# Kernel optimization log

Hardware: AMD Instinct MI355X
Metric: run time of the kernel (lower is better)

Reference implementation:

```python
import jax, jax.numpy as jnp
import numpy as np

B, S, H, NH, FF = 16, 1024, 768, 12, 3072
D = H // NH  # 64
EPS = 1e-12


def layer_norm(x, g, b):
    mu = jnp.mean(x, axis=-1, keepdims=True)
    var = jnp.mean(jnp.square(x - mu), axis=-1, keepdims=True)
    return (x - mu) * jax.lax.rsqrt(var + EPS) * g + b


def setup_inputs() -> dict:
    key = jax.random.key(0)
    ks = jax.random.split(key, 16)
    w = lambda k, shape: (jax.random.normal(k, shape, jnp.float32) * 0.02)
    return {
        "features": jax.random.normal(ks[0], (B, S, H), jnp.float32),
        "attention_mask": jnp.zeros((B, S), jnp.float32),  # additive mask
        "wq": w(ks[1], (H, H)), "bq": jnp.zeros((H,), jnp.float32),
        "wk": w(ks[2], (H, H)), "bk": jnp.zeros((H,), jnp.float32),
        "wv": w(ks[3], (H, H)), "bv": jnp.zeros((H,), jnp.float32),
        "wo": w(ks[4], (H, H)), "bo": jnp.zeros((H,), jnp.float32),
        "ln1_g": jnp.ones((H,), jnp.float32), "ln1_b": jnp.zeros((H,), jnp.float32),
        "w1": w(ks[5], (H, FF)), "b1": jnp.zeros((FF,), jnp.float32),
        "w2": w(ks[6], (FF, H)), "b2": jnp.zeros((H,), jnp.float32),
        "ln2_g": jnp.ones((H,), jnp.float32), "ln2_b": jnp.zeros((H,), jnp.float32),
        "wp": w(ks[7], (H, H)), "bp": jnp.zeros((H,), jnp.float32),
        "wm": w(ks[8], (H, 1)), "bm": jnp.zeros((1,), jnp.float32),
    }


def reference(features, attention_mask, wq, bq, wk, bk, wv, bv, wo, bo,
              ln1_g, ln1_b, w1, b1, w2, b2, ln2_g, ln2_b, wp, bp, wm, bm):
    mask = attention_mask[:, None, None, :]  # [B,1,1,S]

    def split_heads(x):  # [B,S,H] -> [B,NH,S,D]
        return x.reshape(B, S, NH, D).transpose(0, 2, 1, 3)

    q = split_heads(features @ wq + bq)
    k = split_heads(features @ wk + bk)
    v = split_heads(features @ wv + bv)

    scores = jnp.einsum("bhqd,bhkd->bhqk", q, k) / np.sqrt(D).astype(np.float32)
    probs = jax.nn.softmax(scores + mask, axis=-1)  # dropout is identity (eval)
    ctx = jnp.einsum("bhqk,bhkd->bhqd", probs, v)
    ctx = ctx.transpose(0, 2, 1, 3).reshape(B, S, H)

    attn_out = layer_norm(ctx @ wo + bo + features, ln1_g, ln1_b)
    ffn = jax.nn.gelu(attn_out @ w1 + b1, approximate=False) @ w2 + b2
    hidden = layer_norm(ffn + attn_out, ln2_g, ln2_b)

    pooled = jnp.tanh(hidden[:, 0] @ wp + bp)  # BertPooler on [CLS]
    cls = (pooled @ wm + bm).squeeze()  # [B]
    return cls
```

## Files before the change

### kernel.cpp

```cpp
#include <hip/hip_runtime.h>
#include <math.h>

namespace {

constexpr int B  = 16;
constexpr int S  = 1024;
constexpr int H  = 768;
constexpr int NH = 12;
constexpr int DH = 64;
constexpr int FF = 3072;
constexpr int XSPL = 32;
constexpr float EPS = 1e-12f;

__device__ __forceinline__ float waveReduceSum(float v) {
#pragma unroll
    for (int d = 1; d < 64; d <<= 1) v += __shfl_xor(v, d);
    return v;
}

__device__ __forceinline__ float blockReduceSum768(float v, float* red) {
    const int lane = threadIdx.x & 63;
    const int wid  = threadIdx.x >> 6;
    v = waveReduceSum(v);
    __syncthreads();
    if (lane == 0) red[wid] = v;
    __syncthreads();
    float s = 0.f;
#pragma unroll
    for (int w = 0; w < 12; ++w) s += red[w];
    return s;
}

template <int K, int ISPL, int N>
__global__ __launch_bounds__(256) void gemm_partial(
        const float* __restrict__ A, int lda, int jtOfsA,
        const float* __restrict__ W, float* __restrict__ part) {
    constexpr int IR = K / ISPL;
    __shared__ float Asl[B * IR];
    const int jt  = blockIdx.x;
    const int sp  = blockIdx.y;
    const int i0  = sp * IR;
    const int tid = threadIdx.x;

    for (int e = tid; e < B * IR; e += 256) {
        const int b = e / IR, ii = e % IR;
        Asl[e] = A[(size_t)b * lda + (size_t)jt * jtOfsA + i0 + ii];
    }
    __syncthreads();

    const int jl = tid & 63;
    const int bg = tid >> 6;
    const int j  = jt * 64 + jl;
    const float* wp_ = W + (size_t)i0 * N + j;
    const float* a0 = Asl + (bg * 4 + 0) * IR;
    const float* a1 = Asl + (bg * 4 + 1) * IR;
    const float* a2 = Asl + (bg * 4 + 2) * IR;
    const float* a3 = Asl + (bg * 4 + 3) * IR;
    float acc0 = 0.f, acc1 = 0.f, acc2 = 0.f, acc3 = 0.f;
#pragma unroll
    for (int ii = 0; ii < IR; ++ii) {
        const float w = wp_[(size_t)ii * N];
        acc0 += w * a0[ii];
        acc1 += w * a1[ii];
        acc2 += w * a2[ii];
        acc3 += w * a3[ii];
    }
    float* pp = part + ((size_t)sp * B) * N + j;
    pp[(size_t)(bg * 4 + 0) * N] = acc0;
    pp[(size_t)(bg * 4 + 1) * N] = acc1;
    pp[(size_t)(bg * 4 + 2) * N] = acc2;
    pp[(size_t)(bg * 4 + 3) * N] = acc3;
}

template <int K, int ISPL, int N, int RED>
__global__ __launch_bounds__(256) void gemm_partial_red(
        const float* __restrict__ Ain, const float* __restrict__ bias,
        const float* __restrict__ W, float* __restrict__ part) {
    constexpr int IR = K / ISPL;
    __shared__ float Asl[B * IR];
    const int jt  = blockIdx.x;
    const int sp  = blockIdx.y;
    const int i0  = sp * IR;
    const int tid = threadIdx.x;

    for (int e = tid; e < B * IR; e += 256) {
        const int b = e / IR, ii = e % IR;
        float v = bias[i0 + ii];
#pragma unroll
        for (int sp2 = 0; sp2 < RED; ++sp2)
            v += Ain[((size_t)sp2 * B + b) * K + i0 + ii];
        Asl[e] = v;
    }
    __syncthreads();

    const int jl = tid & 63;
    const int bg = tid >> 6;
    const int j  = jt * 64 + jl;
    const float* wp_ = W + (size_t)i0 * N + j;
    const float* a0 = Asl + (bg * 4 + 0) * IR;
    const float* a1 = Asl + (bg * 4 + 1) * IR;
    const float* a2 = Asl + (bg * 4 + 2) * IR;
    const float* a3 = Asl + (bg * 4 + 3) * IR;
    float acc0 = 0.f, acc1 = 0.f, acc2 = 0.f, acc3 = 0.f;
#pragma unroll
    for (int ii = 0; ii < IR; ++ii) {
        const float w = wp_[(size_t)ii * N];
        acc0 += w * a0[ii];
        acc1 += w * a1[ii];
        acc2 += w * a2[ii];
        acc3 += w * a3[ii];
    }
    float* pp = part + ((size_t)sp * B) * N + j;
    pp[(size_t)(bg * 4 + 0) * N] = acc0;
    pp[(size_t)(bg * 4 + 1) * N] = acc1;
    pp[(size_t)(bg * 4 + 2) * N] = acc2;
    pp[(size_t)(bg * 4 + 3) * N] = acc3;
}

template <int K, int ISPL, int N, int RED>
__global__ __launch_bounds__(256) void gemm_partial_red_gelu(
        const float* __restrict__ Ain, const float* __restrict__ bias,
        const float* __restrict__ W, float* __restrict__ part) {
    constexpr int IR = K / ISPL;
    __shared__ float Asl[B * IR];
    const int jt  = blockIdx.x;
    const int sp  = blockIdx.y;
    const int i0  = sp * IR;
    const int tid = threadIdx.x;

    for (int e = tid; e < B * IR; e += 256) {
        const int b = e / IR, ii = e % IR;
        float v = bias[i0 + ii];
#pragma unroll
        for (int sp2 = 0; sp2 < RED; ++sp2)
            v += Ain[((size_t)sp2 * B + b) * K + i0 + ii];
        Asl[e] = 0.5f * v * (1.0f + erff(v * 0.70710678118654752440f));
    }
    __syncthreads();

    const int jl = tid & 63;
    const int bg = tid >> 6;
    const int j  = jt * 64 + jl;
    const float* wp_ = W + (size_t)i0 * N + j;
    const float* a0 = Asl + (bg * 4 + 0) * IR;
    const float* a1 = Asl + (bg * 4 + 1) * IR;
    const float* a2 = Asl + (bg * 4 + 2) * IR;
    const float* a3 = Asl + (bg * 4 + 3) * IR;
    float acc0 = 0.f, acc1 = 0.f, acc2 = 0.f, acc3 = 0.f;
#pragma unroll 32
    for (int ii = 0; ii < IR; ++ii) {
        const float w = wp_[(size_t)ii * N];
        acc0 += w * a0[ii];
        acc1 += w * a1[ii];
        acc2 += w * a2[ii];
        acc3 += w * a3[ii];
    }
    float* pp = part + ((size_t)sp * B) * N + j;
    pp[(size_t)(bg * 4 + 0) * N] = acc0;
    pp[(size_t)(bg * 4 + 1) * N] = acc1;
    pp[(size_t)(bg * 4 + 2) * N] = acc2;
    pp[(size_t)(bg * 4 + 3) * N] = acc3;
}

template <int ISPL>
__global__ __launch_bounds__(256) void gemm_xpart(
        const float* __restrict__ xpart, const float* __restrict__ psum,
        const float* __restrict__ W, float* __restrict__ part) {
    constexpr int IR = H / ISPL;
    __shared__ float Asl[B * IR];
    __shared__ float rinvl[B];
    const int jt  = blockIdx.x;
    const int sp  = blockIdx.y;
    const int i0  = sp * IR;
    const int tid = threadIdx.x;

    if (tid < B) {
        float s = 0.f;
#pragma unroll
        for (int kt = 0; kt < XSPL; ++kt)
            s += psum[((size_t)(tid * XSPL + kt)) * NH + jt];
        rinvl[tid] = 1.0f / s;
    }
    __syncthreads();

    for (int e = tid; e < B * IR; e += 256) {
        const int bb = e / IR, ii = e % IR;
        float v = 0.f;
#pragma unroll
        for (int s2 = 0; s2 < XSPL; ++s2)
            v += xpart[(((size_t)(bb * XSPL + s2)) * NH + jt) * H + i0 + ii];
        Asl[e] = v * rinvl[bb];
    }
    __syncthreads();

    const int jl = tid & 63;
    const int bg = tid >> 6;
    const int j  = jt * 64 + jl;
    const float* wp_ = W + (size_t)i0 * H + j;
    const float* a0 = Asl + (bg * 4 + 0) * IR;
    const float* a1 = Asl + (bg * 4 + 1) * IR;
    const float* a2 = Asl + (bg * 4 + 2) * IR;
    const float* a3 = Asl + (bg * 4 + 3) * IR;
    float acc0 = 0.f, acc1 = 0.f, acc2 = 0.f, acc3 = 0.f;
#pragma unroll
    for (int ii = 0; ii < IR; ++ii) {
        const float w = wp_[(size_t)ii * H];
        acc0 += w * a0[ii];
        acc1 += w * a1[ii];
        acc2 += w * a2[ii];
        acc3 += w * a3[ii];
    }
    float* pp = part + ((size_t)sp * B) * H + j;
    pp[(size_t)(bg * 4 + 0) * H] = acc0;
    pp[(size_t)(bg * 4 + 1) * H] = acc1;
    pp[(size_t)(bg * 4 + 2) * H] = acc2;
    pp[(size_t)(bg * 4 + 3) * H] = acc3;
}

__global__ __launch_bounds__(256) void qu_kernel(
        const float* __restrict__ x, const float* __restrict__ wq,
        const float* __restrict__ bq, const float* __restrict__ wk,
        const float* __restrict__ bk,
        float* __restrict__ u, float* __restrict__ constk) {
    const int b = blockIdx.x / NH, h = blockIdx.x % NH;
    __shared__ float qh[DH];
    __shared__ float red[4][DH];
    const int tid = threadIdx.x;
    const int d = tid & 63, seg = tid >> 6;

    {
        const float* xr  = x + (size_t)b * S * H;
        const float* wqp = wq + (size_t)(seg * 192) * H + h * DH + d;
        float acc = 0.f;
#pragma unroll 8
        for (int i = 0; i < 192; ++i)
            acc += xr[seg * 192 + i] * wqp[(size_t)i * H];
        red[seg][d] = acc;
    }
    __syncthreads();
    if (tid < DH)
        qh[tid] = bq[h * DH + tid] + red[0][tid] + red[1][tid] + red[2][tid] + red[3][tid];
    __syncthreads();
    if (tid < DH) {
        float v = bk[h * DH + tid] * qh[tid];
        v = waveReduceSum(v);
        if (tid == 0) constk[b * NH + h] = v;
    }

    const int jj = tid & 3, iq = tid >> 2;
    const float4* qv = (const float4*)qh;
    float4 q4[4];
#pragma unroll
    for (int c = 0; c < 4; ++c) q4[c] = qv[jj * 4 + c];
#pragma unroll 4
    for (int ir = 0; ir < 12; ++ir) {
        const int i = ir * 64 + iq;
        const float4* wr = (const float4*)(wk + (size_t)i * H + h * DH);
        float s = 0.f;
#pragma unroll
        for (int c = 0; c < 4; ++c) {
            const float4 w = wr[jj * 4 + c];
            s += w.x * q4[c].x + w.y * q4[c].y + w.z * q4[c].z + w.w * q4[c].w;
        }
        s += __shfl_xor(s, 1);
        s += __shfl_xor(s, 2);
        if (jj == 0) u[((size_t)(b * NH + h)) * H + i] = s;
    }
}

__global__ __launch_bounds__(256, 2) void score_xbar_kernel(
        const float* __restrict__ x, const float* __restrict__ u,
        const float* __restrict__ constk, const float* __restrict__ mask,
        float* __restrict__ psum, float* __restrict__ xpart) {
    const int b  = blockIdx.x;
    const int kt = blockIdx.y;
    __shared__ __align__(16) float ul[NH * H];
    __shared__ float ck[NH];
    __shared__ float wsum[4][NH];
    __shared__ __align__(16) float el[32][NH];
    const int tid = threadIdx.x;
    {
        const float4* ug = (const float4*)(u + (size_t)b * NH * H);
        float4* ul4 = (float4*)ul;
        for (int e = tid; e < NH * H / 4; e += 256) ul4[e] = ug[e];
        if (tid < NH) ck[tid] = constk[b * NH + tid];
    }
    __syncthreads();

    const int jj = tid & 15, kk = tid >> 4;
    const int k0 = kt * 32 + kk * 2;
    float4 xv0[12], xv1[12];
    {
        const float4* xr0 = (const float4*)(x + ((size_t)b * S + k0) * H);
        const float4* xr1 = (const float4*)(x + ((size_t)b * S + k0 + 1) * H);
#pragma unroll
        for (int t = 0; t < 12; ++t) { xv0[t] = xr0[jj + 16 * t]; xv1[t] = xr1[jj + 16 * t]; }
    }
    const float4* ul4 = (const float4*)ul;
    float acc0[NH], acc1[NH];
#pragma unroll
    for (int h = 0; h < NH; ++h) {
        float a0 = 0.f, a1 = 0.f;
#pragma unroll
        for (int t = 0; t < 12; ++t) {
            const float4 uv = ul4[h * 192 + jj + 16 * t];
            a0 += xv0[t].x * uv.x + xv0[t].y * uv.y + xv0[t].z * uv.z + xv0[t].w * uv.w;
            a1 += xv1[t].x * uv.x + xv1[t].y * uv.y + xv1[t].z * uv.z + xv1[t].w * uv.w;
        }
        acc0[h] = a0; acc1[h] = a1;
    }
#pragma unroll
    for (int h = 0; h < NH; ++h) {
#pragma unroll
        for (int d = 1; d < 16; d <<= 1) {
            acc0[h] += __shfl_xor(acc0[h], d);
            acc1[h] += __shfl_xor(acc1[h], d);
        }
    }
    const float mk0 = mask[b * S + k0];
    const float mk1 = mask[b * S + k0 + 1];
    float e0[NH], e1[NH], ps[NH];
#pragma unroll
    for (int h = 0; h < NH; ++h) {
        e0[h] = expf(acc0[h] * 0.125f + ck[h] + mk0);
        e1[h] = expf(acc1[h] * 0.125f + ck[h] + mk1);
        ps[h] = e0[h] + e1[h];
    }
    if (jj == 0) {
#pragma unroll
        for (int h = 0; h < NH; ++h) {
            el[kk * 2 + 0][h] = e0[h];
            el[kk * 2 + 1][h] = e1[h];
        }
    }
#pragma unroll
    for (int h = 0; h < NH; ++h) {
        ps[h] += __shfl_xor(ps[h], 16);
        ps[h] += __shfl_xor(ps[h], 32);
    }
    const int wid = tid >> 6;
    if ((tid & 63) == 0) {
#pragma unroll
        for (int h = 0; h < NH; ++h) wsum[wid][h] = ps[h];
    }
    __syncthreads();
    if (tid < NH)
        psum[((size_t)(b * XSPL + kt)) * NH + tid] =
            wsum[0][tid] + wsum[1][tid] + wsum[2][tid] + wsum[3][tid];

    float accx[3][NH];
#pragma unroll
    for (int c = 0; c < 3; ++c)
#pragma unroll
        for (int h = 0; h < NH; ++h) accx[c][h] = 0.f;
    const float* xb = x + ((size_t)b * S + (size_t)kt * 32) * H;
#pragma unroll 8
    for (int k = 0; k < 32; ++k) {
        const float xs0 = xb[(size_t)k * H + tid];
        const float xs1 = xb[(size_t)k * H + tid + 256];
        const float xs2 = xb[(size_t)k * H + tid + 512];
#pragma unroll
        for (int h = 0; h < NH; ++h) {
            const float ee = el[k][h];
            accx[0][h] += ee * xs0;
            accx[1][h] += ee * xs1;
            accx[2][h] += ee * xs2;
        }
    }
    float* op = xpart + ((size_t)(b * XSPL + kt)) * NH * H + tid;
#pragma unroll
    for (int h = 0; h < NH; ++h) {
        op[(size_t)h * H +   0] = accx[0][h];
        op[(size_t)h * H + 256] = accx[1][h];
        op[(size_t)h * H + 512] = accx[2][h];
    }
}

template <int ISPL>
__global__ __launch_bounds__(768) void ln_kernel(
        const float* __restrict__ part, const float* __restrict__ bias,
        const float* __restrict__ resid, int residStride,
        const float* __restrict__ g, const float* __restrict__ bet,
        float* __restrict__ out) {
    __shared__ float red[12];
    const int b = blockIdx.x, j = threadIdx.x;
    float v = bias[j] + resid[(size_t)b * residStride + j];
#pragma unroll
    for (int sp = 0; sp < ISPL; ++sp) v += part[((size_t)sp * B + b) * H + j];
    const float mu = blockReduceSum768(v, red) * (1.0f / H);
    const float d  = v - mu;
    const float var = blockReduceSum768(d * d, red) * (1.0f / H);
    out[(size_t)b * H + j] = d * rsqrtf(var + EPS) * g[j] + bet[j];
}

template <int ISPL>
__global__ __launch_bounds__(768) void cls_kernel(
        const float* __restrict__ part, const float* __restrict__ bp,
        const float* __restrict__ wm, const float* __restrict__ bm,
        float* __restrict__ out) {
    __shared__ float red[12];
    const int b = blockIdx.x, j = threadIdx.x;
    float v = bp[j];
#pragma unroll
    for (int sp = 0; sp < ISPL; ++sp) v += part[((size_t)sp * B + b) * H + j];
    v = tanhf(v);
    const float s = blockReduceSum768(v * wm[j], red);
    if (j == 0) out[b] = s + bm[0];
}

}

extern "C" void kernel_launch(void* const* d_in, const int* in_sizes, int n_in,
                              void* d_out, int out_size, void* d_ws, size_t ws_size,
                              hipStream_t stream) {
    const float* x    = (const float*)d_in[0];
    const float* mask = (const float*)d_in[1];
    const float* wq   = (const float*)d_in[2];
    const float* bq   = (const float*)d_in[3];
    const float* wk   = (const float*)d_in[4];
    const float* bk   = (const float*)d_in[5];
    const float* wv   = (const float*)d_in[6];
    const float* bv   = (const float*)d_in[7];
    const float* wo   = (const float*)d_in[8];
    const float* bo   = (const float*)d_in[9];
    const float* ln1g = (const float*)d_in[10];
    const float* ln1b = (const float*)d_in[11];
    const float* w1   = (const float*)d_in[12];
    const float* b1   = (const float*)d_in[13];
    const float* w2   = (const float*)d_in[14];
    const float* b2   = (const float*)d_in[15];
    const float* ln2g = (const float*)d_in[16];
    const float* ln2b = (const float*)d_in[17];
    const float* wp   = (const float*)d_in[18];
    const float* bp   = (const float*)d_in[19];
    const float* wm   = (const float*)d_in[20];
    const float* bm   = (const float*)d_in[21];
    float* out = (float*)d_out;

    float* ws = (float*)d_ws;
    size_t o = 0;
    float* u        = ws + o; o += (size_t)B * NH * H;
    float* constk   = ws + o; o += 256;
    float* psum     = ws + o; o += (size_t)B * XSPL * NH;
    float* attn_out = ws + o; o += (size_t)B * H;
    float* hidden   = ws + o; o += (size_t)B * H;
    float* arena    = ws + o;
    float* xpart     = arena;
    float* ctx_part  = arena + (size_t)XSPL * B * NH * H;
    float* wo_part   = ctx_part + (size_t)24 * B * H;
    float* ffn1_part = arena;
    float* ffn2_part = arena + (size_t)24 * B * FF;
    float* pool_part = arena;
    (void)ws_size; (void)in_sizes; (void)n_in; (void)out_size;

    qu_kernel<<<B * NH, 256, 0, stream>>>(x, wq, bq, wk, bk, u, constk);

    score_xbar_kernel<<<dim3(B, S / 32), 256, 0, stream>>>(x, u, constk, mask, psum, xpart);

    gemm_xpart<24><<<dim3(12, 24), 256, 0, stream>>>(xpart, psum, wv, ctx_part);

    gemm_partial_red<H, 24, H, 24><<<dim3(12, 24), 256, 0, stream>>>(ctx_part, bv, wo, wo_part);
    ln_kernel<24><<<B, 768, 0, stream>>>(wo_part, bo, x, S * H, ln1g, ln1b, attn_out);

    gemm_partial<H, 24, FF><<<dim3(48, 24), 256, 0, stream>>>(attn_out, H, 0, w1, ffn1_part);
    gemm_partial_red_gelu<FF, 48, H, 24><<<dim3(12, 48), 256, 0, stream>>>(ffn1_part, b1, w2, ffn2_part);
    ln_kernel<48><<<B, 768, 0, stream>>>(ffn2_part, b2, attn_out, H, ln2g, ln2b, hidden);

    gemm_partial<H, 24, H><<<dim3(12, 24), 256, 0, stream>>>(hidden, H, 0, wp, pool_part);
    cls_kernel<24><<<B, 768, 0, stream>>>(pool_part, bp, wm, bm, out);
}
```

Baseline: 217.2 us.

## Split CLS query projection into split-K GEMM, fuse pooler with classifier head

The fused per-(batch,head) query and u kernel is replaced by a split-K partial GEMM for the CLS query projection plus a new u kernel. The new kernel stages a tile of wk in shared memory and reuses it across all 16 batch rows, where before each block re-read wk per batch. The pooler GEMM and classifier are fused into one kernel that does the full 768-length dot product per output, removing a partial-sum buffer and one launch. The score kernel also loads its attention weights as float4 vectors and lowers the unroll factor. The pooler now runs on only 16 blocks, so it trades parallelism for fewer launches.

```diff
diff --git a/kernel.cpp b/kernel.cpp
--- a/kernel.cpp
+++ b/kernel.cpp
@@ -162,6 +162,61 @@
     pp[(size_t)(bg * 4 + 3) * N] = acc3;
 }
 
+__global__ __launch_bounds__(256) void u_kernel3(
+        const float* __restrict__ q0_part, const float* __restrict__ bq,
+        const float* __restrict__ wk, const float* __restrict__ bk,
+        float* __restrict__ u, float* __restrict__ constk) {
+    const int h = blockIdx.x, seg = blockIdx.y;
+    const int i0 = seg * 64;
+    __shared__ float qh[B][DH + 1];
+    __shared__ float wkl[64][DH + 1];
+    const int tid = threadIdx.x;
+
+    for (int e = tid; e < B * DH; e += 256) {
+        const int b = e >> 6, d = e & 63;
+        float v = bq[h * DH + d];
+#pragma unroll
+        for (int sp = 0; sp < 24; ++sp)
+            v += q0_part[((size_t)sp * B + b) * H + h * DH + d];
+        qh[b][d] = v;
+    }
+    {
+        const float4* wg = (const float4*)(wk + (size_t)i0 * H + h * DH);
+        for (int e = tid; e < 64 * 16; e += 256) {
+            const int r = e >> 4, c4 = e & 15;
+            const float4 w = wg[(size_t)r * (H / 4) + c4];
+            wkl[r][c4 * 4 + 0] = w.x;
+            wkl[r][c4 * 4 + 1] = w.y;
+            wkl[r][c4 * 4 + 2] = w.z;
+            wkl[r][c4 * 4 + 3] = w.w;
+        }
+    }
+    __syncthreads();
+
+    if (seg == 0 && tid < B) {
+        float s = 0.f;
+#pragma unroll
+        for (int d = 0; d < DH; ++d) s += bk[h * DH + d] * qh[tid][d];
+        constk[tid * NH + h] = s;
+    }
+
+    const int il = tid & 63;
+    const int bg = tid >> 6;
+    float acc0 = 0.f, acc1 = 0.f, acc2 = 0.f, acc3 = 0.f;
+#pragma unroll
+    for (int d = 0; d < DH; ++d) {
+        const float w = wkl[il][d];
+        acc0 += w * qh[bg * 4 + 0][d];
+        acc1 += w * qh[bg * 4 + 1][d];
+        acc2 += w * qh[bg * 4 + 2][d];
+        acc3 += w * qh[bg * 4 + 3][d];
+    }
+    u[((size_t)((bg * 4 + 0) * NH + h)) * H + i0 + il] = acc0;
+    u[((size_t)((bg * 4 + 1) * NH + h)) * H + i0 + il] = acc1;
+    u[((size_t)((bg * 4 + 2) * NH + h)) * H + i0 + il] = acc2;
+    u[((size_t)((bg * 4 + 3) * NH + h)) * H + i0 + il] = acc3;
+}
+
 template <int ISPL>
 __global__ __launch_bounds__(256) void gemm_xpart(
         const float* __restrict__ xpart, const float* __restrict__ psum,
@@ -217,57 +272,6 @@
     pp[(size_t)(bg * 4 + 3) * H] = acc3;
 }
 
-__global__ __launch_bounds__(256) void qu_kernel(
-        const float* __restrict__ x, const float* __restrict__ wq,
-        const float* __restrict__ bq, const float* __restrict__ wk,
-        const float* __restrict__ bk,
-        float* __restrict__ u, float* __restrict__ constk) {
-    const int b = blockIdx.x / NH, h = blockIdx.x % NH;
-    __shared__ float qh[DH];
-    __shared__ float red[4][DH];
-    const int tid = threadIdx.x;
-    const int d = tid & 63, seg = tid >> 6;
-
-    {
-        const float* xr  = x + (size_t)b * S * H;
-        const float* wqp = wq + (size_t)(seg * 192) * H + h * DH + d;
-        float acc = 0.f;
-#pragma unroll 8
-        for (int i = 0; i < 192; ++i)
-            acc += xr[seg * 192 + i] * wqp[(size_t)i * H];
-        red[seg][d] = acc;
-    }
-    __syncthreads();
-    if (tid < DH)
-        qh[tid] = bq[h * DH + tid] + red[0][tid] + red[1][tid] + red[2][tid] + red[3][tid];
-    __syncthreads();
-    if (tid < DH) {
-        float v = bk[h * DH + tid] * qh[tid];
-        v = waveReduceSum(v);
-        if (tid == 0) constk[b * NH + h] = v;
-    }
-
-    const int jj = tid & 3, iq = tid >> 2;
-    const float4* qv = (const float4*)qh;
-    float4 q4[4];
-#pragma unroll
-    for (int c = 0; c < 4; ++c) q4[c] = qv[jj * 4 + c];
-#pragma unroll 4
-    for (int ir = 0; ir < 12; ++ir) {
-        const int i = ir * 64 + iq;
-        const float4* wr = (const float4*)(wk + (size_t)i * H + h * DH);
-        float s = 0.f;
-#pragma unroll
-        for (int c = 0; c < 4; ++c) {
-            const float4 w = wr[jj * 4 + c];
-            s += w.x * q4[c].x + w.y * q4[c].y + w.z * q4[c].z + w.w * q4[c].w;
-        }
-        s += __shfl_xor(s, 1);
-        s += __shfl_xor(s, 2);
-        if (jj == 0) u[((size_t)(b * NH + h)) * H + i] = s;
-    }
-}
-
 __global__ __launch_bounds__(256, 2) void score_xbar_kernel(
         const float* __restrict__ x, const float* __restrict__ u,
         const float* __restrict__ constk, const float* __restrict__ mask,
@@ -354,17 +358,22 @@
 #pragma unroll
         for (int h = 0; h < NH; ++h) accx[c][h] = 0.f;
     const float* xb = x + ((size_t)b * S + (size_t)kt * 32) * H;
-#pragma unroll 8
+#pragma unroll 4
     for (int k = 0; k < 32; ++k) {
         const float xs0 = xb[(size_t)k * H + tid];
         const float xs1 = xb[(size_t)k * H + tid + 256];
         const float xs2 = xb[(size_t)k * H + tid + 512];
+        const float4 ea = *(const float4*)(&el[k][0]);
+        const float4 eb = *(const float4*)(&el[k][4]);
+        const float4 ec = *(const float4*)(&el[k][8]);
+        const float eh[12] = {ea.x, ea.y, ea.z, ea.w,
+                              eb.x, eb.y, eb.z, eb.w,
+                              ec.x, ec.y, ec.z, ec.w};
 #pragma unroll
         for (int h = 0; h < NH; ++h) {
-            const float ee = el[k][h];
-            accx[0][h] += ee * xs0;
-            accx[1][h] += ee * xs1;
-            accx[2][h] += ee * xs2;
+            accx[0][h] += eh[h] * xs0;
+            accx[1][h] += eh[h] * xs1;
+            accx[2][h] += eh[h] * xs2;
         }
     }
     float* op = xpart + ((size_t)(b * XSPL + kt)) * NH * H + tid;
@@ -393,17 +402,20 @@
     out[(size_t)b * H + j] = d * rsqrtf(var + EPS) * g[j] + bet[j];
 }
 
-template <int ISPL>
-__global__ __launch_bounds__(768) void cls_kernel(
-        const float* __restrict__ part, const float* __restrict__ bp,
-        const float* __restrict__ wm, const float* __restrict__ bm,
-        float* __restrict__ out) {
+__global__ __launch_bounds__(768) void poolcls_kernel(
+        const float* __restrict__ hidden, const float* __restrict__ wp,
+        const float* __restrict__ bp, const float* __restrict__ wm,
+        const float* __restrict__ bm, float* __restrict__ out) {
+    __shared__ float hl[H];
     __shared__ float red[12];
     const int b = blockIdx.x, j = threadIdx.x;
-    float v = bp[j];
-#pragma unroll
-    for (int sp = 0; sp < ISPL; ++sp) v += part[((size_t)sp * B + b) * H + j];
-    v = tanhf(v);
+    hl[j] = hidden[(size_t)b * H + j];
+    __syncthreads();
+    float acc = bp[j];
+#pragma unroll 8
+    for (int i = 0; i < H; ++i)
+        acc += hl[i] * wp[(size_t)i * H + j];
+    const float v = tanhf(acc);
     const float s = blockReduceSum768(v * wm[j], red);
     if (j == 0) out[b] = s + bm[0];
 }
@@ -445,27 +457,22 @@
     float* attn_out = ws + o; o += (size_t)B * H;
     float* hidden   = ws + o; o += (size_t)B * H;
     float* arena    = ws + o;
+    float* q0_part   = arena;
     float* xpart     = arena;
     float* ctx_part  = arena + (size_t)XSPL * B * NH * H;
     float* wo_part   = ctx_part + (size_t)24 * B * H;
     float* ffn1_part = arena;
     float* ffn2_part = arena + (size_t)24 * B * FF;
-    float* pool_part = arena;
     (void)ws_size; (void)in_sizes; (void)n_in; (void)out_size;
 
-    qu_kernel<<<B * NH, 256, 0, stream>>>(x, wq, bq, wk, bk, u, constk);
-
+    gemm_partial<H, 24, H><<<dim3(12, 24), 256, 0, stream>>>(x, S * H, 0, wq, q0_part);
+    u_kernel3<<<dim3(NH, 12), 256, 0, stream>>>(q0_part, bq, wk, bk, u, constk);
     score_xbar_kernel<<<dim3(B, S / 32), 256, 0, stream>>>(x, u, constk, mask, psum, xpart);
-
     gemm_xpart<24><<<dim3(12, 24), 256, 0, stream>>>(xpart, psum, wv, ctx_part);
-
     gemm_partial_red<H, 24, H, 24><<<dim3(12, 24), 256, 0, stream>>>(ctx_part, bv, wo, wo_part);
     ln_kernel<24><<<B, 768, 0, stream>>>(wo_part, bo, x, S * H, ln1g, ln1b, attn_out);
-
     gemm_partial<H, 24, FF><<<dim3(48, 24), 256, 0, stream>>>(attn_out, H, 0, w1, ffn1_part);
     gemm_partial_red_gelu<FF, 48, H, 24><<<dim3(12, 48), 256, 0, stream>>>(ffn1_part, b1, w2, ffn2_part);
     ln_kernel<48><<<B, 768, 0, stream>>>(ffn2_part, b2, attn_out, H, ln2g, ln2b, hidden);
-
-    gemm_partial<H, 24, H><<<dim3(12, 24), 256, 0, stream>>>(hidden, H, 0, wp, pool_part);
-    cls_kernel<24><<<B, 768, 0, stream>>>(pool_part, bp, wm, bm, out);
-}
+    poolcls_kernel<<<B, 768, 0, stream>>>(hidden, wp, bp, wm, bm, out);
+}
```

Result: slower. 251.9 us (+16.0%).
